# Optimization experiments

Measured on AMD Instinct MI355X. Metric: run time of the kernel, lower is better.

## Reference

```python
import jax, jax.numpy as jnp
import numpy as np

B = 4096
UNITS = 2048
INP = 2048


def setup_inputs() -> dict:
    key = jax.random.key(0)
    k1, k2, k3, k4 = jax.random.split(key, 4)
    pre_layer = jax.random.normal(k1, (2, B, UNITS), dtype=jnp.float32)
    x = jax.random.normal(k2, (B, INP), dtype=jnp.float32)
    W = jax.random.normal(k3, (4, UNITS, INP), dtype=jnp.float32) * 0.02
    U = jax.random.normal(k4, (4, UNITS, UNITS), dtype=jnp.float32) * 0.02
    return {"pre_layer": pre_layer, "x": x, "W": W, "U": U}


def reference(pre_layer, x, W, U):
    pre_h, pre_c = pre_layer[0], pre_layer[1]
    # Fuse the 8 matmuls into 2 batched GEMMs: gates[g] = x @ W[g].T + pre_h @ U[g].T
    gates = jnp.einsum('bi,gui->gbu', x, W) + jnp.einsum('bh,guh->gbu', pre_h, U)
    i_t = jax.nn.sigmoid(gates[0])
    f_t = jax.nn.sigmoid(gates[1])
    o_t = jax.nn.sigmoid(gates[2])
    n_c_t = jnp.tanh(gates[3])
    c = f_t * pre_c + i_t * n_c_t
    h = o_t * jnp.tanh(c)
    return jnp.stack([h, c])
```

## Files before the change

kernel.cpp:

```cpp
#include <hip/hip_runtime.h>
#include <hip/hip_bf16.h>

#define B_DIM 4096
#define UNITS_DIM 2048
#define K_DIM 4096
#define M_DIM 8192

typedef __bf16 bf16x8 __attribute__((ext_vector_type(8)));
typedef float f32x4 __attribute__((ext_vector_type(4)));

#define AS1C(p) ((const __attribute__((address_space(1))) void*)(p))
#define AS3(p)  ((__attribute__((address_space(3))) void*)(p))

__device__ __forceinline__ float fast_sigmoid(float x) {
    return 1.0f / (1.0f + __expf(-x));
}
__device__ __forceinline__ float fast_tanh(float x) {
    return 2.0f / (1.0f + __expf(-2.0f * x)) - 1.0f;
}

__global__ void convert_act(const float* __restrict__ pre_h,
                            const float* __restrict__ x,
                            __hip_bfloat16* __restrict__ Abf) {
    const long long idx = (long long)blockIdx.x * blockDim.x + threadIdx.x;
    const long long e = idx * 8;
    const int b = (int)(e >> 12);
    const int k = (int)(e & 4095);
    const float* src = (k < UNITS_DIM)
        ? (x + (long long)b * UNITS_DIM + k)
        : (pre_h + (long long)b * UNITS_DIM + (k - UNITS_DIM));
    float4 f0 = ((const float4*)src)[0];
    float4 f1 = ((const float4*)src)[1];
    union { __hip_bfloat16 h[8]; uint4 u4; } p;
    p.h[0] = __float2bfloat16(f0.x); p.h[1] = __float2bfloat16(f0.y);
    p.h[2] = __float2bfloat16(f0.z); p.h[3] = __float2bfloat16(f0.w);
    p.h[4] = __float2bfloat16(f1.x); p.h[5] = __float2bfloat16(f1.y);
    p.h[6] = __float2bfloat16(f1.z); p.h[7] = __float2bfloat16(f1.w);
    *(uint4*)(Abf + e) = p.u4;
}

__global__ void convert_wu(const float* __restrict__ W,
                           const float* __restrict__ U,
                           __hip_bfloat16* __restrict__ Bbf) {
    const long long idx = (long long)blockIdx.x * blockDim.x + threadIdx.x;
    const long long e = idx * 8;
    const int n = (int)(e >> 12);
    const int k = (int)(e & 4095);
    const int u = n >> 2;
    const int g = n & 3;
    const float* src = (k < UNITS_DIM)
        ? (W + ((long long)g * UNITS_DIM + u) * UNITS_DIM + k)
        : (U + ((long long)g * UNITS_DIM + u) * UNITS_DIM + (k - UNITS_DIM));
    float4 f0 = ((const float4*)src)[0];
    float4 f1 = ((const float4*)src)[1];
    union { __hip_bfloat16 h[8]; uint4 u4; } p;
    p.h[0] = __float2bfloat16(f0.x); p.h[1] = __float2bfloat16(f0.y);
    p.h[2] = __float2bfloat16(f0.z); p.h[3] = __float2bfloat16(f0.w);
    p.h[4] = __float2bfloat16(f1.x); p.h[5] = __float2bfloat16(f1.y);
    p.h[6] = __float2bfloat16(f1.z); p.h[7] = __float2bfloat16(f1.w);
    *(uint4*)(Bbf + e) = p.u4;
}

__global__ __launch_bounds__(256, 3) void lstm_gemm(
    const __hip_bfloat16* __restrict__ Wc,
    const __hip_bfloat16* __restrict__ Ac,
    const float* __restrict__ pre_c,
    float* __restrict__ out)
{
    __shared__ __hip_bfloat16 As[128 * 64];
    __shared__ __hip_bfloat16 Bs[128 * 64];

    const int tid  = threadIdx.x;
    const int lane = tid & 63;
    const int wave = tid >> 6;
    const int m_base = blockIdx.x * 128;
    const int n_base = blockIdx.y * 128;
    const int wm = (wave >> 1) * 64;
    const int wn = (wave & 1) * 64;
    const int l15 = lane & 15;
    const int lq  = lane >> 4;
    const int x7  = l15 & 7;

    f32x4 acc[4][4] = {};

    const int srow = tid >> 3;
    const int scol = (((tid & 7) ^ (srow & 7)) * 8);
    const __hip_bfloat16* wg = Wc + (size_t)(m_base + srow) * K_DIM + scol;
    const __hip_bfloat16* ag = Ac + (size_t)(n_base + srow) * K_DIM + scol;

    for (int k0 = 0; k0 < K_DIM; k0 += 64) {
#pragma unroll
        for (int r = 0; r < 4; ++r) {
            __builtin_amdgcn_global_load_lds(
                AS1C(wg + (size_t)(r * 32) * K_DIM + k0),
                AS3(As + r * 2048 + tid * 8), 16, 0, 0);
            __builtin_amdgcn_global_load_lds(
                AS1C(ag + (size_t)(r * 32) * K_DIM + k0),
                AS3(Bs + r * 2048 + tid * 8), 16, 0, 0);
        }
        __syncthreads();
#pragma unroll
        for (int ki = 0; ki < 2; ++ki) {
            const int ca = ((ki * 4 + lq) ^ x7) * 8;
            bf16x8 af[4], bfr[4];
#pragma unroll
            for (int mi = 0; mi < 4; ++mi)
                af[mi] = *(const bf16x8*)(As + (wm + mi * 16 + l15) * 64 + ca);
#pragma unroll
            for (int ni = 0; ni < 4; ++ni)
                bfr[ni] = *(const bf16x8*)(Bs + (wn + ni * 16 + l15) * 64 + ca);
#pragma unroll
            for (int mi = 0; mi < 4; ++mi)
#pragma unroll
                for (int ni = 0; ni < 4; ++ni)
                    acc[mi][ni] = __builtin_amdgcn_mfma_f32_16x16x32_bf16(
                        af[mi], bfr[ni], acc[mi][ni], 0, 0, 0);
        }
        __syncthreads();
    }

#pragma unroll
    for (int mi = 0; mi < 4; ++mi) {
        const int u = ((m_base + wm + mi * 16) >> 2) + lq;
#pragma unroll
        for (int ni = 0; ni < 4; ++ni) {
            const int b = n_base + wn + ni * 16 + l15;
            f32x4 gv = acc[mi][ni];
            float i_t = fast_sigmoid(gv[0]);
            float f_t = fast_sigmoid(gv[1]);
            float o_t = fast_sigmoid(gv[2]);
            float n_t = fast_tanh(gv[3]);
            float pc  = pre_c[(size_t)b * UNITS_DIM + u];
            float c   = f_t * pc + i_t * n_t;
            float h   = o_t * fast_tanh(c);
            out[(size_t)b * UNITS_DIM + u] = h;
            out[(size_t)B_DIM * UNITS_DIM + (size_t)b * UNITS_DIM + u] = c;
        }
    }
}

extern "C" void kernel_launch(void* const* d_in, const int* in_sizes, int n_in,
                              void* d_out, int out_size, void* d_ws, size_t ws_size,
                              hipStream_t stream) {
    const float* pre_layer = (const float*)d_in[0];
    const float* x         = (const float*)d_in[1];
    const float* W         = (const float*)d_in[2];
    const float* U         = (const float*)d_in[3];
    float* out = (float*)d_out;

    const float* pre_h = pre_layer;
    const float* pre_c = pre_layer + (size_t)B_DIM * UNITS_DIM;

    __hip_bfloat16* Abf = (__hip_bfloat16*)d_ws;
    __hip_bfloat16* Bbf = (__hip_bfloat16*)((char*)d_ws +
                          (size_t)B_DIM * K_DIM * sizeof(__hip_bfloat16));

    convert_act<<<8192, 256, 0, stream>>>(pre_h, x, Abf);
    convert_wu<<<16384, 256, 0, stream>>>(W, U, Bbf);

    dim3 grid(M_DIM / 128, B_DIM / 128);
    lstm_gemm<<<grid, 256, 0, stream>>>(Bbf, Abf, pre_c, out);
}
```

Before: 522.6 us.

## Use 256x256 tiles with 4-stage LDS pipeline and XCD-aware block remap

Replaces the 128x128 single-buffered GEMM tile with a 256x256 tile computed by 512 threads, using a 4-deep ring of LDS buffers with K-step 32 so global loads for three future steps are in flight while MFMAs run. Block indices are remapped so consecutive workgroups on the same XCD share tiles, and wave priority is raised around the MFMA block. This aims to hide global-load latency, halve barriers per FLOP and improve L2 reuse. In exchange it uses 128KB of LDS and more accumulator registers, which lowers occupancy.

```diff
diff --git a/kernel.cpp b/kernel.cpp
--- a/kernel.cpp
+++ b/kernel.cpp
@@ -61,66 +61,97 @@
     *(uint4*)(Bbf + e) = p.u4;
 }
 
-__global__ __launch_bounds__(256, 3) void lstm_gemm(
+__global__ __launch_bounds__(512, 2) void lstm_gemm(
     const __hip_bfloat16* __restrict__ Wc,
     const __hip_bfloat16* __restrict__ Ac,
     const float* __restrict__ pre_c,
     float* __restrict__ out)
 {
-    __shared__ __hip_bfloat16 As[128 * 64];
-    __shared__ __hip_bfloat16 Bs[128 * 64];
+    __shared__ __hip_bfloat16 As[4 * 8192];
+    __shared__ __hip_bfloat16 Bs[4 * 8192];
 
     const int tid  = threadIdx.x;
     const int lane = tid & 63;
     const int wave = tid >> 6;
-    const int m_base = blockIdx.x * 128;
-    const int n_base = blockIdx.y * 128;
-    const int wm = (wave >> 1) * 64;
-    const int wn = (wave & 1) * 64;
+
+    const int bid  = blockIdx.x;
+    const int wgid = (bid & 7) * 64 + (bid >> 3);
+    const int m_base = (wgid & 31) * 256;
+    const int n_base = (wgid >> 5) * 256;
+
+    const int wm  = (wave >> 2) * 128;
+    const int wn  = (wave & 3) * 64;
     const int l15 = lane & 15;
     const int lq  = lane >> 4;
-    const int x7  = l15 & 7;
+    const int keyr = (l15 >> 1) & 3;
 
-    f32x4 acc[4][4] = {};
+    const int aofs = (wm + l15) * 32 + ((lq ^ keyr) * 8);
+    const int bofs = (wn + l15) * 32 + ((lq ^ keyr) * 8);
 
-    const int srow = tid >> 3;
-    const int scol = (((tid & 7) ^ (srow & 7)) * 8);
-    const __hip_bfloat16* wg = Wc + (size_t)(m_base + srow) * K_DIM + scol;
-    const __hip_bfloat16* ag = Ac + (size_t)(n_base + srow) * K_DIM + scol;
+    const int r0 = tid >> 2;
+    const int gc = (((tid & 3) ^ ((tid >> 3) & 3)) * 8);
+    const __hip_bfloat16* wg0 = Wc + (size_t)(m_base + r0) * K_DIM + gc;
+    const __hip_bfloat16* ag0 = Ac + (size_t)(n_base + r0) * K_DIM + gc;
 
-    for (int k0 = 0; k0 < K_DIM; k0 += 64) {
+#define STAGE(T) do {                                                          \
+        const int sb_ = (T) & 3;                                               \
+        const size_t ko_ = (size_t)(T) * 32;                                   \
+        __builtin_amdgcn_global_load_lds(AS1C(wg0 + ko_),                      \
+            AS3(As + sb_ * 8192 + tid * 8), 16, 0, 0);                         \
+        __builtin_amdgcn_global_load_lds(AS1C(wg0 + (size_t)128 * K_DIM + ko_),\
+            AS3(As + sb_ * 8192 + 4096 + tid * 8), 16, 0, 0);                  \
+        __builtin_amdgcn_global_load_lds(AS1C(ag0 + ko_),                      \
+            AS3(Bs + sb_ * 8192 + tid * 8), 16, 0, 0);                         \
+        __builtin_amdgcn_global_load_lds(AS1C(ag0 + (size_t)128 * K_DIM + ko_),\
+            AS3(Bs + sb_ * 8192 + 4096 + tid * 8), 16, 0, 0);                  \
+    } while (0)
+
+    f32x4 acc[8][4] = {};
+
+    STAGE(0);
+    STAGE(1);
+    STAGE(2);
+    asm volatile("s_waitcnt vmcnt(8)" ::: "memory");
+    __builtin_amdgcn_s_barrier();
+
+    for (int t = 0; t < 128; ++t) {
+        const int buf = t & 3;
+        const __hip_bfloat16* Ab = As + buf * 8192 + aofs;
+        const __hip_bfloat16* Bb = Bs + buf * 8192 + bofs;
+        bf16x8 af[8], bfv[4];
 #pragma unroll
-        for (int r = 0; r < 4; ++r) {
-            __builtin_amdgcn_global_load_lds(
-                AS1C(wg + (size_t)(r * 32) * K_DIM + k0),
-                AS3(As + r * 2048 + tid * 8), 16, 0, 0);
-            __builtin_amdgcn_global_load_lds(
-                AS1C(ag + (size_t)(r * 32) * K_DIM + k0),
-                AS3(Bs + r * 2048 + tid * 8), 16, 0, 0);
-        }
-        __syncthreads();
+        for (int mi = 0; mi < 8; ++mi)
+            af[mi] = *(const bf16x8*)(Ab + mi * 512);
 #pragma unroll
-        for (int ki = 0; ki < 2; ++ki) {
-            const int ca = ((ki * 4 + lq) ^ x7) * 8;
-            bf16x8 af[4], bfr[4];
+        for (int ni = 0; ni < 4; ++ni)
+            bfv[ni] = *(const bf16x8*)(Bb + ni * 512);
+
+        if (t < 125) STAGE(t + 3);
+
+        __builtin_amdgcn_sched_barrier(0);
+        asm volatile("s_waitcnt lgkmcnt(0)" ::: "memory");
+        if (t < 125)
+            asm volatile("s_waitcnt vmcnt(8)" ::: "memory");
+        else if (t == 125)
+            asm volatile("s_waitcnt vmcnt(4)" ::: "memory");
+        else
+            asm volatile("s_waitcnt vmcnt(0)" ::: "memory");
+        __builtin_amdgcn_s_barrier();
+        __builtin_amdgcn_sched_barrier(0);
+
+        __builtin_amdgcn_s_setprio(1);
 #pragma unroll
-            for (int mi = 0; mi < 4; ++mi)
-                af[mi] = *(const bf16x8*)(As + (wm + mi * 16 + l15) * 64 + ca);
+        for (int mi = 0; mi < 8; ++mi)
 #pragma unroll
             for (int ni = 0; ni < 4; ++ni)
-                bfr[ni] = *(const bf16x8*)(Bs + (wn + ni * 16 + l15) * 64 + ca);
-#pragma unroll
-            for (int mi = 0; mi < 4; ++mi)
-#pragma unroll
-                for (int ni = 0; ni < 4; ++ni)
-                    acc[mi][ni] = __builtin_amdgcn_mfma_f32_16x16x32_bf16(
-                        af[mi], bfr[ni], acc[mi][ni], 0, 0, 0);
-        }
-        __syncthreads();
+                acc[mi][ni] = __builtin_amdgcn_mfma_f32_16x16x32_bf16(
+                    af[mi], bfv[ni], acc[mi][ni], 0, 0, 0);
+        __builtin_amdgcn_s_setprio(0);
     }
+#undef STAGE
 
 #pragma unroll
-    for (int mi = 0; mi < 4; ++mi) {
+    for (int mi = 0; mi < 8; ++mi) {
         const int u = ((m_base + wm + mi * 16) >> 2) + lq;
 #pragma unroll
         for (int ni = 0; ni < 4; ++ni) {
@@ -158,6 +189,5 @@
     convert_act<<<8192, 256, 0, stream>>>(pre_h, x, Abf);
     convert_wu<<<16384, 256, 0, stream>>>(W, U, Bbf);
 
-    dim3 grid(M_DIM / 128, B_DIM / 128);
-    lstm_gemm<<<grid, 256, 0, stream>>>(Bbf, Abf, pre_c, out);
+    lstm_gemm<<<512, 512, 0, stream>>>(Bbf, Abf, pre_c, out);
 }
```

After: 505.2 us. -3.3%, faster.
